# Optimization experiments

Hardware: AMD Instinct MI355X
Metric: run time of the kernel (lower is better)

## Reference

```python
import jax, jax.numpy as jnp
import numpy as np

NUM_HEADS = 8
CH_PER_HEAD = 32
NUM_GROUPS = 32
EPS = 1e-5
SCALE = CH_PER_HEAD ** (-0.25)


def setup_inputs() -> dict:
    key = jax.random.key(0)
    ks = jax.random.split(key, 6)
    B, C, H, W = 2, 256, 64, 64
    hid = NUM_HEADS * CH_PER_HEAD  # 256
    s = 1.0 / np.sqrt(C)
    return {
        "x": jax.random.normal(ks[0], (B, C, H, W), dtype=jnp.float32),
        "gamma": jnp.ones((C,), jnp.float32),
        "beta": jnp.zeros((C,), jnp.float32),
        "wq": jax.random.normal(ks[1], (hid, C), jnp.float32) * s,
        "bq": jnp.zeros((hid,), jnp.float32),
        "wk": jax.random.normal(ks[2], (hid, C), jnp.float32) * s,
        "bk": jnp.zeros((hid,), jnp.float32),
        "wv": jax.random.normal(ks[3], (hid, C), jnp.float32) * s,
        "bv": jnp.zeros((hid,), jnp.float32),
        "wout": jax.random.normal(ks[4], (C, hid), jnp.float32) * s,
        "bout": jnp.zeros((C,), jnp.float32),
    }


def _group_norm(x, gamma, beta):
    b, c, h, w = x.shape
    xg = x.reshape(b, NUM_GROUPS, c // NUM_GROUPS, h, w)
    mu = jnp.mean(xg, axis=(2, 3, 4), keepdims=True)
    var = jnp.var(xg, axis=(2, 3, 4), keepdims=True)
    xg = (xg - mu) * jax.lax.rsqrt(var + EPS)
    return xg.reshape(b, c, h, w) * gamma[None, :, None, None] + beta[None, :, None, None]


def reference(x, gamma, beta, wq, bq, wk, bk, wv, bv, wout, bout):
    b, c, h, w = x.shape
    n = h * w
    x_n = _group_norm(x, gamma, beta).reshape(b, c, n)  # b c n (self-attention: embedding = x_n)
    # 1x1 convs == pointwise linear over the channel dim
    q = jnp.einsum('oc,bcn->bon', wq, x_n) + bq[None, :, None]
    k = jnp.einsum('oc,bcn->bon', wk, x_n) + bk[None, :, None]
    v = jnp.einsum('oc,bcn->bon', wv, x_n) + bv[None, :, None]
    # split heads: b (h d) n -> b h d n
    d = CH_PER_HEAD
    q = q.reshape(b, NUM_HEADS, d, n)
    k = k.reshape(b, NUM_HEADS, d, n)
    v = v.reshape(b, NUM_HEADS, d, n)
    attn = jax.nn.softmax(jnp.einsum('bhdi,bhdj->bhij', q * SCALE, k * SCALE), axis=-1)
    out = jnp.einsum('bhij,bhdj->bhdi', attn, v).reshape(b, NUM_HEADS * d, n)
    out = jnp.einsum('oc,bcn->bon', wout, out) + bout[None, :, None]
    out = out.reshape(b, -1, h, w)
    return x + out  # shapes match -> residual
```

## Files before the change

### kernel.cpp

```cpp
#include <hip/hip_runtime.h>
#include <hip/hip_bf16.h>
#include <stdint.h>

typedef unsigned short u16;
typedef float f32x4 __attribute__((ext_vector_type(4)));
typedef float f32x16 __attribute__((ext_vector_type(16)));
typedef short bf16x8 __attribute__((ext_vector_type(8)));

#define NSP 4096
#define CDIM 256
#define HID 256
#define NH 8
#define DH 32
#define NG 32
#define CPG 8
#define BATCH 2
#define SPLIT 4
#define GN_EPS 1e-5f
#define QK2_SCALE 0.25503488f

#define MFMA32(A, B, C) __builtin_amdgcn_mfma_f32_32x32x16_bf16(A, B, C, 0, 0, 0)
#define MFMA16(A, B, C) __builtin_amdgcn_mfma_f32_16x16x32_bf16(A, B, C, 0, 0, 0)

__device__ __forceinline__ float bf2f(u16 u) {
    union { uint32_t i; float f; } v; v.i = ((uint32_t)u) << 16; return v.f;
}
__device__ __forceinline__ u16 f2bf(float f) {
    union { float f; uint32_t i; } v; v.f = f;
    uint32_t b = v.i;
    return (u16)((b + 0x7FFFu + ((b >> 16) & 1u)) >> 16);
}

__device__ __forceinline__ void gload16(const u16* g, u16* lds) {
    __builtin_amdgcn_global_load_lds(
        (const __attribute__((address_space(1))) uint32_t*)g,
        (__attribute__((address_space(3))) uint32_t*)lds, 16, 0, 0);
}

__device__ __forceinline__ void pl32swap(uint32_t& a, uint32_t& b) {
    asm("v_permlane32_swap_b32 %0, %1" : "+v"(a), "+v"(b));
}

__global__ __launch_bounds__(256) void stats_partial(
    const float* __restrict__ x, float* __restrict__ partials,
    const float* __restrict__ wq, const float* __restrict__ wk,
    const float* __restrict__ wv, const float* __restrict__ wout,
    u16* __restrict__ wcat) {
    int blk = blockIdx.x;
    int t = threadIdx.x;
#pragma unroll
    for (int i = 0; i < 2; i++) {
        int idx = blk * 512 + i * 256 + t;
        const float* src = (idx < 65536) ? wq : (idx < 131072) ? wk : (idx < 196608) ? wv : wout;
        wcat[idx] = f2bf(src[idx & 65535]);
    }
    int bg = blk >> 3, sl = blk & 7;
    const float4* base = (const float4*)(x + (size_t)bg * (CPG * NSP) + sl * 4096);
    float s = 0.f, ss = 0.f;
#pragma unroll
    for (int i = 0; i < 4; i++) {
        float4 v = base[t + i * 256];
        s  += v.x + v.y + v.z + v.w;
        ss += v.x * v.x + v.y * v.y + v.z * v.z + v.w * v.w;
    }
    for (int m = 1; m < 64; m <<= 1) { s += __shfl_xor(s, m, 64); ss += __shfl_xor(ss, m, 64); }
    __shared__ float ls[4], lss[4];
    int w = t >> 6;
    if ((t & 63) == 0) { ls[w] = s; lss[w] = ss; }
    __syncthreads();
    if (t == 0) {
        partials[bg * 16 + sl * 2]     = ls[0] + ls[1] + ls[2] + ls[3];
        partials[bg * 16 + sl * 2 + 1] = lss[0] + lss[1] + lss[2] + lss[3];
    }
}

__global__ void gn_apply(const float* __restrict__ x, const float* __restrict__ partials,
                         const float* __restrict__ gamma, const float* __restrict__ beta,
                         u16* __restrict__ xn) {
    __shared__ u16 tile[64][72];
    __shared__ float mr[8][2];
    int n0 = blockIdx.x * 64, c0 = blockIdx.y * 64, b = blockIdx.z;
    int t = threadIdx.x;
    if (t < 8) {
        int bg = b * NG + (c0 >> 3) + t;
        float s = 0.f, ss = 0.f;
#pragma unroll
        for (int sl = 0; sl < 8; sl++) {
            s  += partials[bg * 16 + sl * 2];
            ss += partials[bg * 16 + sl * 2 + 1];
        }
        float mean = s * (1.0f / 32768.0f);
        float var = ss * (1.0f / 32768.0f) - mean * mean;
        mr[t][0] = mean;
        mr[t][1] = rsqrtf(var + GN_EPS);
    }
    __syncthreads();
    int nl = t & 63, cq = t >> 6;
#pragma unroll
    for (int i = 0; i < 16; i++) {
        int cl = i * 4 + cq;
        int c = c0 + cl;
        float mean = mr[cl >> 3][0];
        float rstd = mr[cl >> 3][1];
        float v = x[((size_t)b * CDIM + c) * NSP + n0 + nl];
        v = (v - mean) * rstd * gamma[c] + beta[c];
        tile[cl][nl] = f2bf(v);
    }
    __syncthreads();
    int nr = t >> 2, cc = (t & 3) * 16;
    uint4 o0, o1;
    u16* p0 = (u16*)&o0; u16* p1 = (u16*)&o1;
#pragma unroll
    for (int j = 0; j < 8; j++) { p0[j] = tile[cc + j][nr]; p1[j] = tile[cc + 8 + j][nr]; }
    size_t orow = ((size_t)b * NSP + n0 + nr) * CDIM + c0 + cc;
    *(uint4*)(xn + orow) = o0;
    *(uint4*)(xn + orow + 8) = o1;
}

__global__ __launch_bounds__(256) void gemm_qkv(
    const u16* __restrict__ A, const u16* __restrict__ wcat,
    const float* __restrict__ bq, const float* __restrict__ bk, const float* __restrict__ bv,
    u16* __restrict__ qb, u16* __restrict__ kfb, u16* __restrict__ vfb) {
    __shared__ u16 SMEM[128 * 136];
    u16* As = SMEM;
    u16* Bs = SMEM + 8192;
    int bz = blockIdx.z;
    const u16* Ab = A + (size_t)bz * NSP * CDIM;
    int n0 = blockIdx.x * 128, m0 = blockIdx.y * 128;
    int seg = n0 >> 8;
    int t = threadIdx.x, lane = t & 63, w = t >> 6;
    int wr = w >> 1, wc = w & 1;
    f32x4 acc[4][4] = {};

    int srow = w * 8 + (lane >> 3);
    int scol = (lane & 7) * 8;
    const u16* asrc = Ab + (size_t)(m0 + srow) * CDIM + scol;
    const u16* bsrc = wcat + (size_t)(n0 + srow) * CDIM + scol;
    u16* albase = As + w * 512;
    u16* blbase = Bs + w * 512;

    int frow = lane & 15, fcol = (lane >> 4) * 8;

    for (int k0 = 0; k0 < CDIM; k0 += 64) {
        __syncthreads();
#pragma unroll
        for (int ro = 0; ro < 4; ro++) {
            gload16(asrc + (size_t)ro * 32 * CDIM + k0, albase + ro * 2048);
            gload16(bsrc + (size_t)ro * 32 * CDIM + k0, blbase + ro * 2048);
        }
        asm volatile("s_waitcnt vmcnt(0)" ::: "memory");
        __syncthreads();
#pragma unroll
        for (int kk = 0; kk < 2; kk++) {
            bf16x8 af[4], bfv[4];
#pragma unroll
            for (int i = 0; i < 4; i++) {
                af[i]  = *(bf16x8*)&As[(wr * 64 + i * 16 + frow) * 64 + kk * 32 + fcol];
                bfv[i] = *(bf16x8*)&Bs[(wc * 64 + i * 16 + frow) * 64 + kk * 32 + fcol];
            }
#pragma unroll
            for (int i = 0; i < 4; i++)
#pragma unroll
                for (int j = 0; j < 4; j++)
                    acc[i][j] = MFMA16(af[i], bfv[j], acc[i][j]);
        }
    }

    const float* bias = (seg == 0) ? bq : (seg == 1) ? bk : bv;
    int r4 = (lane >> 4) * 4, cx = lane & 15;
    const int STR = 136;
    __syncthreads();

    if (seg <= 1) {
#pragma unroll
        for (int i = 0; i < 4; i++) {
            int row_l = wr * 64 + i * 16 + r4;
#pragma unroll
            for (int j = 0; j < 4; j++) {
                int col_l = wc * 64 + j * 16 + cx;
                float bb = bias[(n0 & 255) + col_l];
#pragma unroll
                for (int r = 0; r < 4; r++) {
                    float vv = acc[i][j][r] + bb;
                    if (seg == 1) vv *= QK2_SCALE;
                    SMEM[(row_l + r) * STR + col_l] = f2bf(vv);
                }
            }
        }
        __syncthreads();
        if (seg == 0) {
#pragma unroll
            for (int i = 0; i < 8; i++) {
                int c = i * 256 + t;
                int row = c >> 4, o = c & 15;
                uint4 v = *(uint4*)&SMEM[row * STR + o * 8];
                *(uint4*)(qb + (size_t)bz * NSP * HID + (size_t)(m0 + row) * HID + (n0 & 255) + o * 8) = v;
            }
        } else {
#pragma unroll
            for (int i = 0; i < 8; i++) {
                int c = i * 256 + t;
                int rl = c & 127, o = c >> 7;
                int colg = (n0 & 255) + o * 8;
                int h2 = colg >> 5;
                int rg = m0 + rl;
                int f = 2 * ((rg >> 5) & 1) + ((colg >> 4) & 1);
                size_t off = ((size_t)(bz * NH + h2) * 64 + (rg >> 6)) * 2048 + (size_t)f * 512
                           + (size_t)(rg & 31) * 8 + (size_t)((colg >> 3) & 1) * 256;
                *(uint4*)(kfb + off) = *(uint4*)&SMEM[rl * STR + o * 8];
            }
        }
    } else {
#pragma unroll
        for (int i = 0; i < 4; i++) {
            int row_l = wr * 64 + i * 16 + r4;
#pragma unroll
            for (int j = 0; j < 4; j++) {
                int col_l = wc * 64 + j * 16 + cx;
                float bb = bias[(n0 & 255) + col_l];
                uint2 pk2;
                pk2.x = ((uint32_t)f2bf(acc[i][j][1] + bb) << 16) | f2bf(acc[i][j][0] + bb);
                pk2.y = ((uint32_t)f2bf(acc[i][j][3] + bb) << 16) | f2bf(acc[i][j][2] + bb);
                *(uint2*)&SMEM[col_l * STR + row_l] = pk2;
            }
        }
        __syncthreads();
#pragma unroll
        for (int i = 0; i < 8; i++) {
            int c = i * 256 + t;
            int dl = c & 127, jl = c >> 7;
            int colg = (n0 & 255) + dl;
            int h2 = colg >> 5, d = colg & 31;
            int ng = m0 + jl * 8;
            int jc = (ng >> 3) & 7;
            size_t off = ((size_t)(bz * NH + h2) * 64 + (ng >> 6)) * 2048 + (size_t)(jc >> 1) * 512
                       + (size_t)(d + (jc & 1) * 32) * 8;
            *(uint4*)(vfb + off) = *(uint4*)&SMEM[dl * STR + jl * 8];
        }
    }
}

__global__ __launch_bounds__(256) void gemm_out(
    const u16* __restrict__ A,
    const u16* __restrict__ B, long sB,
    const float* __restrict__ bias,
    const float* __restrict__ resid, long sR,
    float* __restrict__ outp, long sO,
    int N) {
    __shared__ u16 As[64][72];
    __shared__ u16 Bs[64][72];
    int bz = blockIdx.z;
    B += (size_t)bz * sB;
    int m0 = blockIdx.y * 64, n0 = blockIdx.x * 64;
    int t = threadIdx.x, lane = t & 63, w = t >> 6;
    int wm = (w >> 1) * 32, wn = (w & 1) * 32;
    f32x4 acc[2][2] = {};

    int sr = t >> 2;
    int sc1 = (t & 3) * 8, sc2 = sc1 + 32;

    uint4 av0 = *(const uint4*)(A + (size_t)(m0 + sr) * CDIM + sc1);
    uint4 av1 = *(const uint4*)(A + (size_t)(m0 + sr) * CDIM + sc2);
    uint4 bv0 = *(const uint4*)(B + (size_t)(n0 + sr) * CDIM + sc1);
    uint4 bv1 = *(const uint4*)(B + (size_t)(n0 + sr) * CDIM + sc2);

    for (int k0 = 0; k0 < CDIM; k0 += 64) {
        __syncthreads();
        *(uint4*)&As[sr][sc1] = av0;
        *(uint4*)&As[sr][sc2] = av1;
        *(uint4*)&Bs[sr][sc1] = bv0;
        *(uint4*)&Bs[sr][sc2] = bv1;
        __syncthreads();
        if (k0 + 64 < CDIM) {
            av0 = *(const uint4*)(A + (size_t)(m0 + sr) * CDIM + k0 + 64 + sc1);
            av1 = *(const uint4*)(A + (size_t)(m0 + sr) * CDIM + k0 + 64 + sc2);
            bv0 = *(const uint4*)(B + (size_t)(n0 + sr) * CDIM + k0 + 64 + sc1);
            bv1 = *(const uint4*)(B + (size_t)(n0 + sr) * CDIM + k0 + 64 + sc2);
        }
#pragma unroll
        for (int ks = 0; ks < 2; ks++) {
            bf16x8 af[2], bfr[2];
#pragma unroll
            for (int i = 0; i < 2; i++) {
                af[i]  = *(bf16x8*)&As[wm + i * 16 + (lane & 15)][ks * 32 + (lane >> 4) * 8];
                bfr[i] = *(bf16x8*)&Bs[wn + i * 16 + (lane & 15)][ks * 32 + (lane >> 4) * 8];
            }
#pragma unroll
            for (int i = 0; i < 2; i++)
#pragma unroll
                for (int j = 0; j < 2; j++)
                    acc[i][j] = MFMA16(af[i], bfr[j], acc[i][j]);
        }
    }

    int r4 = (lane >> 4) * 4, cx = lane & 15;
#pragma unroll
    for (int i = 0; i < 2; i++)
#pragma unroll
        for (int j = 0; j < 2; j++) {
            int rbase = m0 + wm + i * 16 + r4;
            int cbase = n0 + wn + j * 16 + cx;
#pragma unroll
            for (int r = 0; r < 4; r++) {
                int row = rbase + r, col = cbase;
                outp[(size_t)bz * sO + (size_t)row * N + col] =
                    acc[i][j][r] + bias[row] + resid[(size_t)bz * sR + (size_t)row * N + col];
            }
        }
}

__global__ __launch_bounds__(256, 3) void attn_kernel(
    const u16* __restrict__ q, const u16* __restrict__ kfb,
    const u16* __restrict__ vfb, u16* __restrict__ po, float* __restrict__ zz) {
    __shared__ float Ls[4][64];
    int h = blockIdx.y;
    int bz = blockIdx.z;
    int b = bz / SPLIT, sp = bz % SPLIT;
    int kv0 = sp * (NSP / SPLIT);
    int t = threadIdx.x, lane = t & 63, w = t >> 6;
    int ql = lane & 31, hi = lane >> 5;
    int q0 = blockIdx.x * 256 + w * 64;

    const u16* qbp = q + (size_t)b * NSP * HID + (size_t)(q0 + ql) * HID + h * DH + hi * 8;
    bf16x8 qa0 = *(const bf16x8*)(qbp);
    bf16x8 qa1 = *(const bf16x8*)(qbp + 16);
    bf16x8 qb0 = *(const bf16x8*)(qbp + 32 * HID);
    bf16x8 qb1 = *(const bf16x8*)(qbp + 32 * HID + 16);

    size_t tbase = ((size_t)(b * NH + h) * 64 + (kv0 >> 6)) * 2048 + (size_t)lane * 8;
    const u16* kp = kfb + tbase;
    const u16* vp = vfb + tbase;

#define LOADKF(kd, it) { \
    kd[0] = *(const bf16x8*)(kp + (size_t)(it) * 2048);        \
    kd[1] = *(const bf16x8*)(kp + (size_t)(it) * 2048 + 512);  \
    kd[2] = *(const bf16x8*)(kp + (size_t)(it) * 2048 + 1024); \
    kd[3] = *(const bf16x8*)(kp + (size_t)(it) * 2048 + 1536); }
#define LOADVF(vd, it) { \
    vd[0] = *(const bf16x8*)(vp + (size_t)(it) * 2048);        \
    vd[1] = *(const bf16x8*)(vp + (size_t)(it) * 2048 + 512);  \
    vd[2] = *(const bf16x8*)(vp + (size_t)(it) * 2048 + 1024); \
    vd[3] = *(const bf16x8*)(vp + (size_t)(it) * 2048 + 1536); }

    f32x16 kzero = {};
    f32x16 oacc_a = {}, oacc_b = {};
    float la0 = 0.f, la1 = 0.f, lb0 = 0.f, lb1 = 0.f;

    auto softpv = [&](f32x16& st, const bf16x8 (&vf)[4], int tt, f32x16& oacc,
                      float& l0, float& l1) {
        uint32_t pk[8];
#pragma unroll
        for (int j = 0; j < 8; j++) {
            float p0 = __builtin_amdgcn_exp2f(st[2 * j]);
            float p1 = __builtin_amdgcn_exp2f(st[2 * j + 1]);
            float ps = p0 + p1;
            if (j & 1) l1 += ps; else l0 += ps;
            uint32_t dd;
            asm("v_cvt_pk_bf16_f32 %0, %1, %2" : "=v"(dd) : "v"(p0), "v"(p1));
            pk[j] = dd;
        }
#pragma unroll
        for (int c = 0; c < 2; c++) {
            uint32_t a0 = pk[4 * c + 0], b0 = pk[4 * c + 2];
            uint32_t a1 = pk[4 * c + 1], b1 = pk[4 * c + 3];
            pl32swap(a0, b0);
            pl32swap(a1, b1);
            union { uint32_t u[4]; bf16x8 v8; } fr;
            fr.u[0] = a0; fr.u[1] = a1; fr.u[2] = b0; fr.u[3] = b1;
            __builtin_amdgcn_s_setprio(1);
            oacc = MFMA32(fr.v8, vf[2 * tt + c], oacc);
            __builtin_amdgcn_s_setprio(0);
        }
    };

    auto process = [&](const bf16x8 (&kf)[4], const bf16x8 (&vf)[4]) {
#pragma unroll
        for (int tt = 0; tt < 2; tt++) {
            __builtin_amdgcn_s_setprio(1);
            f32x16 st_a = MFMA32(kf[2 * tt], qa0, kzero);
            st_a = MFMA32(kf[2 * tt + 1], qa1, st_a);
            f32x16 st_b = MFMA32(kf[2 * tt], qb0, kzero);
            st_b = MFMA32(kf[2 * tt + 1], qb1, st_b);
            __builtin_amdgcn_s_setprio(0);
            softpv(st_a, vf, tt, oacc_a, la0, la1);
            softpv(st_b, vf, tt, oacc_b, lb0, lb1);
        }
    };

    const int NT = (NSP / SPLIT) / 64;
    bf16x8 k0[4], v0[4], k1[4], v1[4];
    LOADKF(k0, 0); LOADVF(v0, 0);
    LOADKF(k1, 1); LOADVF(v1, 1);
    for (int it = 0; it < NT; it += 2) {
        process(k0, v0);
        int n2 = (it + 2 < NT) ? it + 2 : 0;
        LOADKF(k0, n2); LOADVF(v0, n2);
        process(k1, v1);
        int n3 = (it + 3 < NT) ? it + 3 : 0;
        LOADKF(k1, n3); LOADVF(v1, n3);
    }
#undef LOADKF
#undef LOADVF

    float la = la0 + la1;
    float lb = lb0 + lb1;
    la += __shfl_xor(la, 32);
    lb += __shfl_xor(lb, 32);
    Ls[w][ql] = 1.0f / la;
    Ls[w][32 + ql] = 1.0f / lb;
    if (hi == 0) {
        zz[(((size_t)bz * NH + h) * NSP) + q0 + ql] = __log2f(la);
        zz[(((size_t)bz * NH + h) * NSP) + q0 + 32 + ql] = __log2f(lb);
    }
    u16* pob = po + ((((size_t)bz * NH + h) * NSP) + q0) * DH + ql;
#pragma unroll
    for (int r = 0; r < 16; r++) {
        int qq = (r & 3) + 8 * (r >> 2) + 4 * hi;
        pob[(size_t)qq * DH] = f2bf(oacc_a[r] * Ls[w][qq]);
        pob[(size_t)(32 + qq) * DH] = f2bf(oacc_b[r] * Ls[w][32 + qq]);
    }
}

__global__ __launch_bounds__(256) void combine_kernel(
    const u16* __restrict__ po, const float* __restrict__ zz, u16* __restrict__ ao) {
    int idx = blockIdx.x * 256 + threadIdx.x;
    int c8 = idx & 31;
    int n  = (idx >> 5) & (NSP - 1);
    int b  = idx >> 17;
    int h  = c8 >> 2;
    int dp = (c8 & 3) * 8;

    float z[SPLIT];
    size_t base[SPLIT];
    float M = -3e38f;
#pragma unroll
    for (int s = 0; s < SPLIT; s++) {
        base[s] = ((((size_t)(b * SPLIT + s) * NH + h) * NSP) + n);
        z[s] = zz[base[s]];
        M = fmaxf(M, z[s]);
    }
    float wsum = 0.f, acc[8] = {};
#pragma unroll
    for (int s = 0; s < SPLIT; s++) {
        float ww = __builtin_amdgcn_exp2f(z[s] - M);
        wsum += ww;
        uint4 o = *(const uint4*)(po + base[s] * DH + dp);
        const u16* op = (const u16*)&o;
#pragma unroll
        for (int j = 0; j < 8; j++) acc[j] += bf2f(op[j]) * ww;
    }
    float inv = 1.0f / wsum;
    uint4 r;
    u16* rp = (u16*)&r;
#pragma unroll
    for (int j = 0; j < 8; j++) rp[j] = f2bf(acc[j] * inv);
    *(uint4*)(ao + (((size_t)b * NSP + n) * HID) + h * DH + dp) = r;
}

extern "C" void kernel_launch(void* const* d_in, const int* in_sizes, int n_in,
                              void* d_out, int out_size, void* d_ws, size_t ws_size,
                              hipStream_t stream) {
    const float* x     = (const float*)d_in[0];
    const float* gamma = (const float*)d_in[1];
    const float* beta  = (const float*)d_in[2];
    const float* wq    = (const float*)d_in[3];
    const float* bq    = (const float*)d_in[4];
    const float* wk    = (const float*)d_in[5];
    const float* bk    = (const float*)d_in[6];
    const float* wv    = (const float*)d_in[7];
    const float* bv    = (const float*)d_in[8];
    const float* wout  = (const float*)d_in[9];
    const float* bout  = (const float*)d_in[10];
    float* out = (float*)d_out;

    char* ws = (char*)d_ws;
    float* partials = (float*)ws;
    u16* wq_b = (u16*)(ws + 4096);
    u16* wo_b = wq_b + 3 * 65536;
    u16* xn = wo_b + 65536;
    u16* qb = xn + (size_t)BATCH * NSP * CDIM;
    u16* kfb = qb + (size_t)BATCH * NSP * HID;
    u16* vfb = kfb + (size_t)BATCH * NH * 64 * 2048;
    u16* aob = vfb + (size_t)BATCH * NH * 64 * 2048;
    u16* pob = aob + (size_t)BATCH * NSP * HID;
    float* zzb = (float*)(pob + (size_t)SPLIT * BATCH * NH * NSP * DH);

    const long sQ = (long)NSP * HID;
    const long sOut = (long)CDIM * NSP;

    stats_partial<<<512, 256, 0, stream>>>(x, partials, wq, wk, wv, wout, wq_b);
    gn_apply<<<dim3(NSP / 64, CDIM / 64, BATCH), 256, 0, stream>>>(x, partials, gamma, beta, xn);

    gemm_qkv<<<dim3(768 / 128, NSP / 128, BATCH), 256, 0, stream>>>(
        xn, wq_b, bq, bk, bv, qb, kfb, vfb);

    attn_kernel<<<dim3(NSP / 256, NH, BATCH * SPLIT), 256, 0, stream>>>(qb, kfb, vfb, pob, zzb);
    combine_kernel<<<(BATCH * NSP * HID / 8) / 256, 256, 0, stream>>>(pob, zzb, aob);

    gemm_out<<<dim3(NSP / 64, CDIM / 64, BATCH), 256, 0, stream>>>(
        wo_b, aob, sQ, bout, x, sOut, out, sOut, NSP);
}
```

Before: 83.59 us.

## Fuse split-KV softmax combine into output projection GEMM B-tile loads

Removes the separate combine kernel and computes the log-sum-exp merge of the four split-KV partial outputs directly while loading the B operand tiles of the output projection GEMM. This drops one launch and the write/read round trip of the combined attention output. In exchange, each gemm_out block (4 along M) redoes the combine for its columns, so the partial outputs are read and merged four times. The B loads are also no longer prefetched one iteration ahead, which exposes their latency.

```diff
diff --git a/kernel.cpp b/kernel.cpp
--- a/kernel.cpp
+++ b/kernel.cpp
@@ -242,7 +242,7 @@
 
 __global__ __launch_bounds__(256) void gemm_out(
     const u16* __restrict__ A,
-    const u16* __restrict__ B, long sB,
+    const u16* __restrict__ po, const float* __restrict__ zz,
     const float* __restrict__ bias,
     const float* __restrict__ resid, long sR,
     float* __restrict__ outp, long sO,
@@ -250,7 +250,6 @@
     __shared__ u16 As[64][72];
     __shared__ u16 Bs[64][72];
     int bz = blockIdx.z;
-    B += (size_t)bz * sB;
     int m0 = blockIdx.y * 64, n0 = blockIdx.x * 64;
     int t = threadIdx.x, lane = t & 63, w = t >> 6;
     int wm = (w >> 1) * 32, wn = (w & 1) * 32;
@@ -258,13 +257,46 @@
 
     int sr = t >> 2;
     int sc1 = (t & 3) * 8, sc2 = sc1 + 32;
+    int nrow = n0 + sr;
+    const size_t SSTRIDE = (size_t)NH * NSP;
+
+    auto cmb = [&](int c) -> uint4 {
+        int h = c >> 5, d = c & 31;
+        size_t zb = (((size_t)(bz * SPLIT) * NH + h) * NSP) + nrow;
+        float z0 = zz[zb];
+        float z1 = zz[zb + SSTRIDE];
+        float z2 = zz[zb + 2 * SSTRIDE];
+        float z3 = zz[zb + 3 * SSTRIDE];
+        float M = fmaxf(fmaxf(z0, z1), fmaxf(z2, z3));
+        float w0 = __builtin_amdgcn_exp2f(z0 - M);
+        float w1 = __builtin_amdgcn_exp2f(z1 - M);
+        float w2 = __builtin_amdgcn_exp2f(z2 - M);
+        float w3 = __builtin_amdgcn_exp2f(z3 - M);
+        float inv = 1.0f / (w0 + w1 + w2 + w3);
+        uint4 o0 = *(const uint4*)(po + zb * DH + d);
+        uint4 o1 = *(const uint4*)(po + (zb + SSTRIDE) * DH + d);
+        uint4 o2 = *(const uint4*)(po + (zb + 2 * SSTRIDE) * DH + d);
+        uint4 o3 = *(const uint4*)(po + (zb + 3 * SSTRIDE) * DH + d);
+        const u16* p0 = (const u16*)&o0;
+        const u16* p1 = (const u16*)&o1;
+        const u16* p2 = (const u16*)&o2;
+        const u16* p3 = (const u16*)&o3;
+        uint4 r;
+        u16* rp = (u16*)&r;
+#pragma unroll
+        for (int j = 0; j < 8; j++) {
+            float a = (bf2f(p0[j]) * w0 + bf2f(p1[j]) * w1 + bf2f(p2[j]) * w2 + bf2f(p3[j]) * w3) * inv;
+            rp[j] = f2bf(a);
+        }
+        return r;
+    };
 
     uint4 av0 = *(const uint4*)(A + (size_t)(m0 + sr) * CDIM + sc1);
     uint4 av1 = *(const uint4*)(A + (size_t)(m0 + sr) * CDIM + sc2);
-    uint4 bv0 = *(const uint4*)(B + (size_t)(n0 + sr) * CDIM + sc1);
-    uint4 bv1 = *(const uint4*)(B + (size_t)(n0 + sr) * CDIM + sc2);
 
     for (int k0 = 0; k0 < CDIM; k0 += 64) {
+        uint4 bv0 = cmb(k0 + sc1);
+        uint4 bv1 = cmb(k0 + sc2);
         __syncthreads();
         *(uint4*)&As[sr][sc1] = av0;
         *(uint4*)&As[sr][sc2] = av1;
@@ -274,8 +306,6 @@
         if (k0 + 64 < CDIM) {
             av0 = *(const uint4*)(A + (size_t)(m0 + sr) * CDIM + k0 + 64 + sc1);
             av1 = *(const uint4*)(A + (size_t)(m0 + sr) * CDIM + k0 + 64 + sc2);
-            bv0 = *(const uint4*)(B + (size_t)(n0 + sr) * CDIM + k0 + 64 + sc1);
-            bv1 = *(const uint4*)(B + (size_t)(n0 + sr) * CDIM + k0 + 64 + sc2);
         }
 #pragma unroll
         for (int ks = 0; ks < 2; ks++) {
@@ -419,42 +449,6 @@
         pob[(size_t)qq * DH] = f2bf(oacc_a[r] * Ls[w][qq]);
         pob[(size_t)(32 + qq) * DH] = f2bf(oacc_b[r] * Ls[w][32 + qq]);
     }
-}
-
-__global__ __launch_bounds__(256) void combine_kernel(
-    const u16* __restrict__ po, const float* __restrict__ zz, u16* __restrict__ ao) {
-    int idx = blockIdx.x * 256 + threadIdx.x;
-    int c8 = idx & 31;
-    int n  = (idx >> 5) & (NSP - 1);
-    int b  = idx >> 17;
-    int h  = c8 >> 2;
-    int dp = (c8 & 3) * 8;
-
-    float z[SPLIT];
-    size_t base[SPLIT];
-    float M = -3e38f;
-#pragma unroll
-    for (int s = 0; s < SPLIT; s++) {
-        base[s] = ((((size_t)(b * SPLIT + s) * NH + h) * NSP) + n);
-        z[s] = zz[base[s]];
-        M = fmaxf(M, z[s]);
-    }
-    float wsum = 0.f, acc[8] = {};
-#pragma unroll
-    for (int s = 0; s < SPLIT; s++) {
-        float ww = __builtin_amdgcn_exp2f(z[s] - M);
-        wsum += ww;
-        uint4 o = *(const uint4*)(po + base[s] * DH + dp);
-        const u16* op = (const u16*)&o;
-#pragma unroll
-        for (int j = 0; j < 8; j++) acc[j] += bf2f(op[j]) * ww;
-    }
-    float inv = 1.0f / wsum;
-    uint4 r;
-    u16* rp = (u16*)&r;
-#pragma unroll
-    for (int j = 0; j < 8; j++) rp[j] = f2bf(acc[j] * inv);
-    *(uint4*)(ao + (((size_t)b * NSP + n) * HID) + h * DH + dp) = r;
 }
 
 extern "C" void kernel_launch(void* const* d_in, const int* in_sizes, int n_in,
@@ -485,7 +479,6 @@
     u16* pob = aob + (size_t)BATCH * NSP * HID;
     float* zzb = (float*)(pob + (size_t)SPLIT * BATCH * NH * NSP * DH);
 
-    const long sQ = (long)NSP * HID;
     const long sOut = (long)CDIM * NSP;
 
     stats_partial<<<512, 256, 0, stream>>>(x, partials, wq, wk, wv, wout, wq_b);
@@ -495,8 +488,7 @@
         xn, wq_b, bq, bk, bv, qb, kfb, vfb);
 
     attn_kernel<<<dim3(NSP / 256, NH, BATCH * SPLIT), 256, 0, stream>>>(qb, kfb, vfb, pob, zzb);
-    combine_kernel<<<(BATCH * NSP * HID / 8) / 256, 256, 0, stream>>>(pob, zzb, aob);
 
     gemm_out<<<dim3(NSP / 64, CDIM / 64, BATCH), 256, 0, stream>>>(
-        wo_b, aob, sQ, bout, x, sOut, out, sOut, NSP);
-}
+        wo_b, pob, zzb, bout, x, sOut, out, sOut, NSP);
+}
```

Result: no change. 82.14 us (-1.7%).
